# Performance work log

Hardware: AMD Instinct MI355X
Metric: run time of the kernel (lower is better)

Reference implementation:

```python
import math
import jax, jax.numpy as jnp
import numpy as np

HIDDEN = 1024
HEADS = 16
HEAD_DIM = HIDDEN // HEADS  # 64
SEQ = 4096
PATCH = 4064  # num rotated (patch) tokens; last PATCH positions get RoPE
EPS = 1e-6


def setup_inputs() -> dict:
    key = jax.random.key(0)
    ks = jax.random.split(key, 8)
    return {
        "x": jax.random.normal(ks[0], (1, SEQ, HIDDEN), dtype=jnp.float32),
        "rope_cos": jax.random.uniform(ks[1], (PATCH, HEAD_DIM // 2), dtype=jnp.float32),
        "rope_sin": jax.random.uniform(ks[2], (PATCH, HEAD_DIM // 2), dtype=jnp.float32),
        "wq": jax.random.normal(ks[3], (HIDDEN, HIDDEN), dtype=jnp.float32) / math.sqrt(HIDDEN),
        "wk": jax.random.normal(ks[4], (HIDDEN, HIDDEN), dtype=jnp.float32) / math.sqrt(HIDDEN),
        "wv": jax.random.normal(ks[5], (HIDDEN, HIDDEN), dtype=jnp.float32) / math.sqrt(HIDDEN),
        "wo": jax.random.normal(ks[6], (HIDDEN, HIDDEN), dtype=jnp.float32) / math.sqrt(HIDDEN),
        "q_norm_w": jnp.ones((HEAD_DIM,), dtype=jnp.float32),
        "k_norm_w": jnp.ones((HEAD_DIM,), dtype=jnp.float32),
    }


def _rms_norm(t, w):
    # RMSNorm over the last (head_dim) axis
    return t * jax.lax.rsqrt(jnp.mean(t * t, axis=-1, keepdims=True) + EPS) * w


def _apply_rope(t, cos, sin):
    # t: [b, s, h, d]; rotate only the last PATCH positions, pairwise complex mul
    b, s, h, d = t.shape
    P = cos.shape[0]
    tail = t[:, s - P:].reshape(b, P, h, d // 2, 2)
    x0, x1 = tail[..., 0], tail[..., 1]
    c = cos[None, :, None, :]
    sn = sin[None, :, None, :]
    rot = jnp.stack([x0 * c - x1 * sn, x0 * sn + x1 * c], axis=-1).reshape(b, P, h, d)
    return jnp.concatenate([t[:, : s - P], rot], axis=1)


def reference(x, rope_cos, rope_sin, wq, wk, wv, wo, q_norm_w, k_norm_w):
    b, s, _ = x.shape
    q = (x @ wq.T).reshape(b, s, HEADS, HEAD_DIM)
    k = (x @ wk.T).reshape(b, s, HEADS, HEAD_DIM)
    v = (x @ wv.T).reshape(b, s, HEADS, HEAD_DIM)
    q = _rms_norm(q, q_norm_w)
    k = _rms_norm(k, k_norm_w)
    q = _apply_rope(q, rope_cos, rope_sin)
    k = _apply_rope(k, rope_cos, rope_sin)
    q = q / math.sqrt(HEAD_DIM)
    scores = jnp.einsum('bqhd,bkhd->bhqk', q, k)
    attn = jax.nn.softmax(scores.astype(jnp.float32), axis=-1)
    out = jnp.einsum('bhqk,bkhd->bqhd', attn, v).reshape(b, s, HIDDEN)
    return out @ wo.T
```

## Files before the change

### kernel.cpp

```cpp
#include <hip/hip_runtime.h>
#include <hip/hip_bf16.h>
#include <stdint.h>

#define HIDDEN 1024
#define HEADS 16
#define HEAD_DIM 64
#define SEQ 4096
#define PATCH 4064
#define SKIP 32

typedef __attribute__((ext_vector_type(8))) short bf16x8;
typedef __attribute__((ext_vector_type(4))) float f32x4;
typedef __attribute__((ext_vector_type(2))) float f32x2;
typedef __attribute__((ext_vector_type(16))) float f32x16;

__device__ __forceinline__ float b2f(unsigned short u){
  union{uint32_t i; float f;} c; c.i = ((uint32_t)u)<<16; return c.f;
}
__device__ __forceinline__ unsigned short f2b(float f){
  union{float f; uint32_t i;} c; c.f=f;
  uint32_t r = c.i + 0x7fffu + ((c.i>>16)&1u);
  return (unsigned short)(r>>16);
}
__device__ __forceinline__ uint32_t cvtpk(float a, float b){
  uint32_t r;
  asm("v_cvt_pk_bf16_f32 %0, %1, %2" : "=v"(r) : "v"(a), "v"(b));
  return r;
}

#define GLD16(gp, lp) __builtin_amdgcn_global_load_lds( \
    (const __attribute__((address_space(1))) void*)(gp), \
    (__attribute__((address_space(3))) void*)(lp), 16, 0, 0)

__global__ __launch_bounds__(256) void convert_all(
    const float* __restrict__ x,  const float* __restrict__ wq,
    const float* __restrict__ wk, const float* __restrict__ wv,
    const float* __restrict__ wo,
    unsigned short* __restrict__ xb,  unsigned short* __restrict__ wqb,
    unsigned short* __restrict__ wkb, unsigned short* __restrict__ wvb,
    unsigned short* __restrict__ wob)
{
  size_t u = (size_t)blockIdx.x*256 + threadIdx.x;
  size_t e = u*8;
  const float* src; unsigned short* dst; size_t off;
  if      (e < 4194304ull) { src=x;  dst=xb;  off=e;            }
  else if (e < 5242880ull) { src=wq; dst=wqb; off=e-4194304ull; }
  else if (e < 6291456ull) { src=wk; dst=wkb; off=e-5242880ull; }
  else if (e < 7340032ull) { src=wv; dst=wvb; off=e-6291456ull; }
  else                     { src=wo; dst=wob; off=e-7340032ull; }
  float4 v0 = *(const float4*)(src+off);
  float4 v1 = *(const float4*)(src+off+4);
  union { bf16x8 v; unsigned short h[8]; } o;
  o.h[0]=f2b(v0.x); o.h[1]=f2b(v0.y); o.h[2]=f2b(v0.z); o.h[3]=f2b(v0.w);
  o.h[4]=f2b(v1.x); o.h[5]=f2b(v1.y); o.h[6]=f2b(v1.z); o.h[7]=f2b(v1.w);
  *(bf16x8*)(dst+off) = o.v;
}

__global__ __launch_bounds__(256) void gemm_qkv(
    const unsigned short* __restrict__ A,
    const unsigned short* __restrict__ B0,
    const unsigned short* __restrict__ B1,
    const unsigned short* __restrict__ B2,
    unsigned short* __restrict__ qout, unsigned short* __restrict__ kout,
    unsigned short* __restrict__ vout,
    const float* __restrict__ rc, const float* __restrict__ rs,
    const float* __restrict__ qw, const float* __restrict__ kw,
    int M, int Nper, int K)
{
  __shared__ unsigned short smem[16384];
  const int tid = threadIdx.x;
  const int w = tid>>6, l = tid&63;
  const int wm = w>>1, wn = w&1;
  const int g = l>>4, lr = l&15;
  const int bm = blockIdx.x;
  int bn = blockIdx.y;
  const int tilesPer = Nper >> 7;
  const int sel = bn / tilesPer;
  bn -= sel*tilesPer;
  const unsigned short* Bsel = (sel==0) ? B0 : ((sel==1) ? B1 : B2);

  const int off0 = w*1024 + l*16;
  const int r0 = off0>>6, c0 = (off0&63)>>1;
  const int off1 = off0 + 4096;
  const int r1 = off1>>6, c1 = (off1&63)>>1;

  const unsigned short* Ab = A    + (size_t)(bm*128)*K;
  const unsigned short* Bb = Bsel + (size_t)(bn*128)*K;

#define STG(db, kt) do { \
    GLD16(Ab + (size_t)r0*K + (kt) + c0, (char*)smem + (db) + off0); \
    GLD16(Ab + (size_t)r1*K + (kt) + c1, (char*)smem + (db) + off1); \
    GLD16(Bb + (size_t)r0*K + (kt) + c0, (char*)smem + (db) + 8192 + off0); \
    GLD16(Bb + (size_t)r1*K + (kt) + c1, (char*)smem + (db) + 8192 + off1); } while(0)

  f32x4 zero = {0.f,0.f,0.f,0.f};
  f32x4 acc[4][4];
  #pragma unroll
  for (int m=0;m<4;m++)
    #pragma unroll
    for (int n=0;n<4;n++) acc[m][n]=zero;

  const int nkt = K >> 5;
  STG(0, 0);
  for (int t = 0; t < nkt; ++t) {
    __syncthreads();
    const int db = (t&1)<<14;
    if (t+1 < nkt) STG(db^16384, (t+1)*32);
    bf16x8 a[4], b[4];
    #pragma unroll
    for (int m=0;m<4;m++)
      a[m] = *(const bf16x8*)((char*)smem + db + (wm*64 + m*16 + lr)*64 + g*16);
    #pragma unroll
    for (int n=0;n<4;n++)
      b[n] = *(const bf16x8*)((char*)smem + db + 8192 + (wn*64 + n*16 + lr)*64 + g*16);
    #pragma unroll
    for (int m=0;m<4;m++)
      #pragma unroll
      for (int n=0;n<4;n++)
        acc[m][n] = __builtin_amdgcn_mfma_f32_16x16x32_bf16(a[m], b[n], acc[m][n], 0,0,0);
  }
#undef STG

  if (sel <= 1) {
    const float* nw = (sel==0) ? qw : kw;
    unsigned short* dst = (sel==0) ? qout : kout;
    const float scl = (sel==0) ? 0.18033688011112042f : 1.0f;
    float wl[4];
    #pragma unroll
    for (int n=0;n<4;n++) wl[n] = nw[n*16+lr];
    const int hglob = bn*2 + wn;
    #pragma unroll
    for (int m=0;m<4;m++){
      const int rowb = bm*128 + wm*64 + m*16 + g*4;
      float rn[4];
      #pragma unroll
      for (int r=0;r<4;r++){
        float ss = 0.f;
        #pragma unroll
        for (int n=0;n<4;n++) ss += acc[m][n][r]*acc[m][n][r];
        ss += __shfl_xor(ss,1); ss += __shfl_xor(ss,2);
        ss += __shfl_xor(ss,4); ss += __shfl_xor(ss,8);
        rn[r] = rsqrtf(ss*(1.f/64.f) + 1e-6f);
      }
      #pragma unroll
      for (int r=0;r<4;r++){
        const int row = rowb + r;
        const int p = row - SKIP;
        #pragma unroll
        for (int n=0;n<4;n++){
          float v = acc[m][n][r]*rn[r]*wl[n];
          float c = 1.f, sn = 0.f;
          if (p >= 0){
            const int d2 = (n*16+lr)>>1;
            c  = rc[p*(HEAD_DIM/2) + d2];
            sn = rs[p*(HEAD_DIM/2) + d2];
          }
          const float partner = __shfl_xor(v, 1);
          const float o2 = (lr&1) ? (partner*sn + v*c) : (v*c - partner*sn);
          dst[(size_t)row*HIDDEN + hglob*64 + n*16 + lr] = f2b(o2*scl);
        }
      }
    }
  } else {
    #pragma unroll
    for (int m=0;m<4;m++){
      const int row = bm*128 + wm*64 + m*16 + g*4;
      #pragma unroll
      for (int n=0;n<4;n++){
        const int col = bn*128 + wn*64 + n*16 + lr;
        #pragma unroll
        for (int r=0;r<4;r++)
          vout[(size_t)(row+r)*HIDDEN + col] = f2b(acc[m][n][r]);
      }
    }
  }
}

__global__ __launch_bounds__(256) void gemm_out(
    const unsigned short* __restrict__ A,
    const unsigned short* __restrict__ B,
    float* __restrict__ Cf, int M, int N, int K)
{
  __shared__ unsigned short smem[12288];
  const int tid = threadIdx.x;
  const int w = tid>>6, l = tid&63;
  const int wm = w>>1, wn = w&1;
  const int g = l>>4, lr = l&15;
  const int bm = blockIdx.x;
  const int bn = blockIdx.y;

  const int off0 = w*1024 + l*16;
  const int r0 = off0>>6, c0 = (off0&63)>>1;
  const int off1 = off0 + 4096;
  const int r1 = off1>>6, c1 = (off1&63)>>1;
  const int offB = tid*16;
  const int rB = offB>>6, cB = (offB&63)>>1;

  const unsigned short* Ab = A + (size_t)(bm*128)*K;
  const unsigned short* Bb = B + (size_t)(bn*64)*K;

#define STG(db, kt) do { \
    GLD16(Ab + (size_t)r0*K + (kt) + c0, (char*)smem + (db) + off0); \
    GLD16(Ab + (size_t)r1*K + (kt) + c1, (char*)smem + (db) + off1); \
    GLD16(Bb + (size_t)rB*K + (kt) + cB, (char*)smem + (db) + 8192 + offB); } while(0)

  f32x4 zero = {0.f,0.f,0.f,0.f};
  f32x4 acc[4][2];
  #pragma unroll
  for (int m=0;m<4;m++)
    #pragma unroll
    for (int n=0;n<2;n++) acc[m][n]=zero;

  const int nkt = K >> 5;
  STG(0, 0);
  for (int t = 0; t < nkt; ++t) {
    __syncthreads();
    const int db = (t&1)*12288;
    if (t+1 < nkt) STG(db^12288, (t+1)*32);
    bf16x8 a[4], b[2];
    #pragma unroll
    for (int m=0;m<4;m++)
      a[m] = *(const bf16x8*)((char*)smem + db + (wm*64 + m*16 + lr)*64 + g*16);
    #pragma unroll
    for (int n=0;n<2;n++)
      b[n] = *(const bf16x8*)((char*)smem + db + 8192 + (wn*32 + n*16 + lr)*64 + g*16);
    #pragma unroll
    for (int m=0;m<4;m++)
      #pragma unroll
      for (int n=0;n<2;n++)
        acc[m][n] = __builtin_amdgcn_mfma_f32_16x16x32_bf16(a[m], b[n], acc[m][n], 0,0,0);
  }
#undef STG

  #pragma unroll
  for (int m=0;m<4;m++){
    const int row = bm*128 + wm*64 + m*16 + g*4;
    #pragma unroll
    for (int n=0;n<2;n++){
      const int col = bn*64 + wn*32 + n*16 + lr;
      #pragma unroll
      for (int r=0;r<4;r++)
        Cf[(size_t)(row+r)*N + col] = acc[m][n][r];
    }
  }
}

__global__ __launch_bounds__(256) void transpose_v(
    const unsigned short* __restrict__ v, unsigned short* __restrict__ vt)
{
  __shared__ unsigned short t[64*72];
  const int h = blockIdx.y;
  const int s0 = blockIdx.x * 64;
  const int tid = threadIdx.x;
  #pragma unroll
  for (int i=0;i<2;i++){
    const int e = tid + i*256;
    const int r = e>>3, cc = (e&7)*8;
    *(bf16x8*)&t[r*72+cc] = *(const bf16x8*)(v + (size_t)(s0+r)*HIDDEN + h*HEAD_DIM + cc);
  }
  __syncthreads();
  #pragma unroll
  for (int i=0;i<2;i++){
    const int e = tid + i*256;
    const int d = e>>3, sc = (e&7)*8;
    union { bf16x8 v8; unsigned short h8[8]; } o;
    #pragma unroll
    for (int j=0;j<8;j++){
      const int x  = sc + j;
      const int px = (x & ~12) | ((x&4)<<1) | ((x&8)>>1);
      o.h8[j] = t[px*72 + d];
    }
    *(bf16x8*)(vt + (size_t)(h*HEAD_DIM + d)*SEQ + s0 + sc) = o.v8;
  }
}

__device__ __forceinline__ void softmax_pack(f32x16 (&st)[2], f32x2 &lacc, bf16x8 (&pf)[4]){
  float pv[32];
  #pragma unroll
  for (int i=0;i<16;i++){
    pv[i]    = __builtin_amdgcn_exp2f(st[0][i]);
    pv[16+i] = __builtin_amdgcn_exp2f(st[1][i]);
  }
  #pragma unroll
  for (int i=0;i<8;i++){
    f32x2 a; a.x = pv[2*i];    a.y = pv[2*i+1];    lacc += a;
    f32x2 b; b.x = pv[16+2*i]; b.y = pv[16+2*i+1]; lacc += b;
  }
  #pragma unroll
  for (int t2=0; t2<2; t2++)
    #pragma unroll
    for (int e=0; e<2; e++){
      union { uint32_t u4[4]; bf16x8 v8; } pu;
      #pragma unroll
      for (int u=0; u<4; u++)
        pu.u4[u] = cvtpk(pv[t2*16+e*8+2*u], pv[t2*16+e*8+2*u+1]);
      pf[2*t2+e] = pu.v8;
    }
}

__global__ __launch_bounds__(256, 2) void attn_kernel(
    const unsigned short* __restrict__ q, const unsigned short* __restrict__ k,
    const unsigned short* __restrict__ vt, unsigned short* __restrict__ po,
    float* __restrict__ lbuf)
{
  __shared__ unsigned short smem[32768];
  const int fid = blockIdx.x + 16*(blockIdx.y + 16*blockIdx.z);
  const int h    = (fid&7)*2 + ((fid>>3)&1);
  const int rem  = fid>>4;
  const int q0   = (rem&15)*256;
  const int half = rem>>4;
  const int tid = threadIdx.x;
  const int w = tid>>6, l = tid&63;
  const int hi = l>>5, lo = l&31;
  const int NT = SEQ/128/2;
  const int tbase = half * NT;

  int kcol[4], vcol[4], vrow[4];
  #pragma unroll
  for (int i=0;i<4;i++){
    const int c = tid + i*256;
    const int rk = c>>3;
    kcol[i] = ((c&7)*16) ^ ((rk&7)<<4);
    const int rv = c>>4;
    vrow[i] = rv;
    vcol[i] = (((c&7)*16) ^ ((rv&7)<<4)) + ((c>>3)&1)*128;
  }
  const unsigned short* kPtr[4]; const unsigned short* vPtr[4];
  #pragma unroll
  for (int i=0;i<4;i++){
    kPtr[i] = k  + (size_t)((tid + i*256)>>3)*HIDDEN + h*HEAD_DIM + (kcol[i]>>1);
    vPtr[i] = vt + ((size_t)(h*HEAD_DIM + vrow[i]))*SEQ + (vcol[i]>>1);
  }

#define STAGE(b, kOffE, vOffE) do { \
    GLD16(kPtr[0] + (kOffE), (char*)smem + (b)*32768 + (tid      )*16); \
    GLD16(kPtr[1] + (kOffE), (char*)smem + (b)*32768 + (tid+ 256 )*16); \
    GLD16(kPtr[2] + (kOffE), (char*)smem + (b)*32768 + (tid+ 512 )*16); \
    GLD16(kPtr[3] + (kOffE), (char*)smem + (b)*32768 + (tid+ 768 )*16); \
    GLD16(vPtr[0] + (vOffE), (char*)smem + (b)*32768 + 16384 + (tid      )*16); \
    GLD16(vPtr[1] + (vOffE), (char*)smem + (b)*32768 + 16384 + (tid+ 256 )*16); \
    GLD16(vPtr[2] + (vOffE), (char*)smem + (b)*32768 + 16384 + (tid+ 512 )*16); \
    GLD16(vPtr[3] + (vOffE), (char*)smem + (b)*32768 + 16384 + (tid+ 768 )*16); \
  } while(0)

  const int swz = (lo&7)<<4;
  int colo[4];
  #pragma unroll
  for (int ks=0; ks<4; ks++) colo[ks] = ((2*ks+hi)*16) ^ swz;

  bf16x8 qf0[4], qf1[4];
  {
    const unsigned short* qp = q + (size_t)(q0 + w*64 + lo)*HIDDEN + h*HEAD_DIM;
    #pragma unroll
    for (int ks=0; ks<4; ks++){
      qf0[ks] = *(const bf16x8*)(qp + ks*16 + hi*8);
      qf1[ks] = *(const bf16x8*)(qp + 32*HIDDEN + ks*16 + hi*8);
    }
  }

  f32x16 ot0[2], ot1[2];
  #pragma unroll
  for (int m2=0;m2<2;m2++)
    #pragma unroll
    for (int i=0;i<16;i++){ ot0[m2][i] = 0.f; ot1[m2][i] = 0.f; }
  f32x2 lacc0 = {0.f,0.f}, lacc1 = {0.f,0.f};

  STAGE(0, (size_t)tbase*128*HIDDEN, (size_t)tbase*128);

  for (int t = 0; t < NT; ++t) {
    __syncthreads();
    if (t+1 < NT) {
      const size_t ta = (size_t)(tbase + t + 1);
      STAGE((t+1)&1, ta*128*HIDDEN, ta*128);
    }
    const char* Kb = (const char*)smem + (t&1)*32768;
    const char* Vb = Kb + 16384;

    f32x16 sA0[2], sA1[2], sB0[2], sB1[2];
    __builtin_amdgcn_s_setprio(1);
    #pragma unroll
    for (int c=0;c<2;c++){
      #pragma unroll
      for (int i=0;i<16;i++){ sA0[c][i]=0.f; sA1[c][i]=0.f; sB0[c][i]=0.f; sB1[c][i]=0.f; }
      #pragma unroll
      for (int ks=0; ks<4; ks++){
        bf16x8 a0 = *(const bf16x8*)(Kb + (32*c+lo)*128 + colo[ks]);
        sA0[c] = __builtin_amdgcn_mfma_f32_32x32x16_bf16(a0, qf0[ks], sA0[c], 0,0,0);
        sA1[c] = __builtin_amdgcn_mfma_f32_32x32x16_bf16(a0, qf1[ks], sA1[c], 0,0,0);
      }
      #pragma unroll
      for (int ks=0; ks<4; ks++){
        bf16x8 a1 = *(const bf16x8*)(Kb + 8192 + (32*c+lo)*128 + colo[ks]);
        sB0[c] = __builtin_amdgcn_mfma_f32_32x32x16_bf16(a1, qf0[ks], sB0[c], 0,0,0);
        sB1[c] = __builtin_amdgcn_mfma_f32_32x32x16_bf16(a1, qf1[ks], sB1[c], 0,0,0);
      }
    }
    __builtin_amdgcn_s_setprio(0);

    bf16x8 pf0[4], pf1[4];
    softmax_pack(sA0, lacc0, pf0);
    softmax_pack(sA1, lacc1, pf1);

    __builtin_amdgcn_s_setprio(1);
    #pragma unroll
    for (int m2=0;m2<2;m2++)
      #pragma unroll
      for (int ks=0; ks<4; ks++){
        bf16x8 a = *(const bf16x8*)(Vb + (32*m2+lo)*256 + colo[ks]);
        ot0[m2] = __builtin_amdgcn_mfma_f32_32x32x16_bf16(a, pf0[ks], ot0[m2], 0,0,0);
        ot1[m2] = __builtin_amdgcn_mfma_f32_32x32x16_bf16(a, pf1[ks], ot1[m2], 0,0,0);
      }
    __builtin_amdgcn_s_setprio(0);

    bf16x8 pg0[4], pg1[4];
    softmax_pack(sB0, lacc0, pg0);
    softmax_pack(sB1, lacc1, pg1);

    __builtin_amdgcn_s_setprio(1);
    #pragma unroll
    for (int m2=0;m2<2;m2++)
      #pragma unroll
      for (int ks=0; ks<4; ks++){
        bf16x8 a = *(const bf16x8*)(Vb + (32*m2+lo)*256 + 128 + colo[ks]);
        ot0[m2] = __builtin_amdgcn_mfma_f32_32x32x16_bf16(a, pg0[ks], ot0[m2], 0,0,0);
        ot1[m2] = __builtin_amdgcn_mfma_f32_32x32x16_bf16(a, pg1[ks], ot1[m2], 0,0,0);
      }
    __builtin_amdgcn_s_setprio(0);
  }

  {
    float ls0 = lacc0.x + lacc0.y;
    ls0 += __shfl_xor(ls0, 32);
    float ls1 = lacc1.x + lacc1.y;
    ls1 += __shfl_xor(ls1, 32);
    if (hi == 0){
      lbuf[(size_t)half*HEADS*SEQ + h*SEQ + q0 + w*64 + lo]      = ls0;
      lbuf[(size_t)half*HEADS*SEQ + h*SEQ + q0 + w*64 + 32 + lo] = ls1;
    }
  }

  __syncthreads();
  #pragma unroll
  for (int m2=0;m2<2;m2++)
    #pragma unroll
    for (int f=0; f<4; f++)
      #pragma unroll
      for (int u=0; u<2; u++){
        const int d = 32*m2 + 8*f + 4*hi + 2*u;
        const uint32_t w0 = cvtpk(ot0[m2][4*f+2*u], ot0[m2][4*f+2*u+1]);
        *(uint32_t*)((char*)smem + (w*64+lo)*128 + ((d*2) ^ swz)) = w0;
        const uint32_t w1 = cvtpk(ot1[m2][4*f+2*u], ot1[m2][4*f+2*u+1]);
        *(uint32_t*)((char*)smem + (w*64+32+lo)*128 + ((d*2) ^ swz)) = w1;
      }
  __syncthreads();
  unsigned short* pout = po + (size_t)half*SEQ*HIDDEN;
  #pragma unroll
  for (int rr=0; rr<2; rr++){
    const int ql = rr*128 + (tid>>1), xh = tid&1;
    #pragma unroll
    for (int i=0;i<4;i++){
      const int cb = xh*64 + i*16;
      bf16x8 vv = *(const bf16x8*)((const char*)smem + ql*128 + (cb ^ ((ql&7)<<4)));
      *(bf16x8*)(pout + (size_t)(q0+ql)*HIDDEN + h*HEAD_DIM + (cb>>1)) = vv;
    }
  }
#undef STAGE
}

__global__ __launch_bounds__(256) void combine_halves(
    const unsigned short* __restrict__ po, const float* __restrict__ lbuf,
    unsigned short* __restrict__ at)
{
  const size_t e = ((size_t)blockIdx.x*256 + threadIdx.x)*8;
  const int qrow = (int)(e >> 10);
  const int h = (int)((e >> 6) & 15);
  const float li = 1.0f / (lbuf[h*SEQ + qrow] + lbuf[HEADS*SEQ + h*SEQ + qrow]);
  union { bf16x8 v; unsigned short s[8]; } a, b, o;
  a.v = *(const bf16x8*)(po + e);
  b.v = *(const bf16x8*)(po + (size_t)SEQ*HIDDEN + e);
  #pragma unroll
  for (int j=0;j<8;j++)
    o.s[j] = f2b((b2f(a.s[j]) + b2f(b.s[j])) * li);
  *(bf16x8*)(at + e) = o.v;
}

extern "C" void kernel_launch(void* const* d_in, const int* in_sizes, int n_in,
                              void* d_out, int out_size, void* d_ws, size_t ws_size,
                              hipStream_t stream)
{
  const float* x  = (const float*)d_in[0];
  const float* rc = (const float*)d_in[1];
  const float* rs = (const float*)d_in[2];
  const float* wq = (const float*)d_in[3];
  const float* wk = (const float*)d_in[4];
  const float* wv = (const float*)d_in[5];
  const float* wo = (const float*)d_in[6];
  const float* qw = (const float*)d_in[7];
  const float* kw = (const float*)d_in[8];
  float* out = (float*)d_out;

  char* ws = (char*)d_ws;
  const size_t MB = 1024*1024;
  unsigned short* xb  = (unsigned short*)(ws + 0);
  unsigned short* wqb = (unsigned short*)(ws + 8*MB);
  unsigned short* wkb = (unsigned short*)(ws + 10*MB);
  unsigned short* wvb = (unsigned short*)(ws + 12*MB);
  unsigned short* wob = (unsigned short*)(ws + 14*MB);
  unsigned short* qkv = (unsigned short*)(ws + 16*MB);
  unsigned short* qb = qkv;
  unsigned short* kb = qkv + (size_t)SEQ*HIDDEN;
  unsigned short* vb = qkv + (size_t)2*SEQ*HIDDEN;
  unsigned short* vt = (unsigned short*)(ws + 0);
  float*          lbuf = (float*)(ws + 8*MB);
  unsigned short* po = (unsigned short*)(ws + 32*MB);
  unsigned short* at = (unsigned short*)(ws + 40*MB);

  convert_all<<<4096, 256, 0, stream>>>(x, wq, wk, wv, wo, xb, wqb, wkb, wvb, wob);
  gemm_qkv<<<dim3(32,24), 256, 0, stream>>>(
      xb, wqb, wkb, wvb, qb, kb, vb, rc, rs, qw, kw, SEQ, HIDDEN, HIDDEN);
  transpose_v<<<dim3(64,16), 256, 0, stream>>>(vb, vt);
  attn_kernel<<<dim3(16,16,2), 256, 0, stream>>>(qb, kb, vt, po, lbuf);
  combine_halves<<<2048, 256, 0, stream>>>(po, lbuf, at);
  gemm_out<<<dim3(32,16), 256, 0, stream>>>(at, wob, out, SEQ, HIDDEN, HIDDEN);
}
```

Before: 174.2 us.

## Split KV halves within one 512-thread block and combine in shared memory

The attention kernel now runs both key-sequence halves inside a single 512-thread workgroup. Each 256-thread half streams 64-key tiles through its own double buffer, and the two partial outputs and row sums are merged through LDS. This removes the separate combine_halves launch and the global round trip for the partial outputs and row sums. In exchange, the grid halves to 256 workgroups at one block per CU, and the per-iteration tile shrinks from 128 to 64 keys, which doubles the number of barriers per key processed.

```diff
diff --git a/kernel.cpp b/kernel.cpp
--- a/kernel.cpp
+++ b/kernel.cpp
@@ -298,49 +298,38 @@
     }
 }
 
-__global__ __launch_bounds__(256, 2) void attn_kernel(
+__global__ __launch_bounds__(512, 1) void attn_kernel(
     const unsigned short* __restrict__ q, const unsigned short* __restrict__ k,
-    const unsigned short* __restrict__ vt, unsigned short* __restrict__ po,
-    float* __restrict__ lbuf)
+    const unsigned short* __restrict__ vt, unsigned short* __restrict__ at)
 {
   __shared__ unsigned short smem[32768];
-  const int fid = blockIdx.x + 16*(blockIdx.y + 16*blockIdx.z);
-  const int h    = (fid&7)*2 + ((fid>>3)&1);
-  const int rem  = fid>>4;
-  const int q0   = (rem&15)*256;
-  const int half = rem>>4;
+  __shared__ float lsm[512];
+  const int fid = blockIdx.x + 16*blockIdx.y;
+  const int h  = (fid&7)*2 + ((fid>>3)&1);
+  const int q0 = (fid>>4)*256;
   const int tid = threadIdx.x;
-  const int w = tid>>6, l = tid&63;
+  const int half = tid>>8;
+  const int ht = tid&255;
+  const int w = (tid>>6)&3, l = tid&63;
   const int hi = l>>5, lo = l&31;
-  const int NT = SEQ/128/2;
-  const int tbase = half * NT;
-
-  int kcol[4], vcol[4], vrow[4];
-  #pragma unroll
-  for (int i=0;i<4;i++){
-    const int c = tid + i*256;
-    const int rk = c>>3;
-    kcol[i] = ((c&7)*16) ^ ((rk&7)<<4);
-    const int rv = c>>4;
-    vrow[i] = rv;
-    vcol[i] = (((c&7)*16) ^ ((rv&7)<<4)) + ((c>>3)&1)*128;
-  }
-  const unsigned short* kPtr[4]; const unsigned short* vPtr[4];
-  #pragma unroll
-  for (int i=0;i<4;i++){
-    kPtr[i] = k  + (size_t)((tid + i*256)>>3)*HIDDEN + h*HEAD_DIM + (kcol[i]>>1);
-    vPtr[i] = vt + ((size_t)(h*HEAD_DIM + vrow[i]))*SEQ + (vcol[i]>>1);
-  }
+  const int NT = 32;
+  const int tbase = half*NT;
+  const int hbase = half*32768;
+
+  const int cA = ht, cB = ht + 256;
+  const int rA = cA>>3, rB = cB>>3;
+  const int colA = ((cA&7)*16) ^ ((rA&7)<<4);
+  const int colB = ((cB&7)*16) ^ ((rB&7)<<4);
+  const unsigned short* kA = k  + (size_t)rA*HIDDEN + h*HEAD_DIM + (colA>>1);
+  const unsigned short* kB = k  + (size_t)rB*HIDDEN + h*HEAD_DIM + (colB>>1);
+  const unsigned short* vA = vt + ((size_t)(h*HEAD_DIM + rA))*SEQ + (colA>>1);
+  const unsigned short* vB = vt + ((size_t)(h*HEAD_DIM + rB))*SEQ + (colB>>1);
 
 #define STAGE(b, kOffE, vOffE) do { \
-    GLD16(kPtr[0] + (kOffE), (char*)smem + (b)*32768 + (tid      )*16); \
-    GLD16(kPtr[1] + (kOffE), (char*)smem + (b)*32768 + (tid+ 256 )*16); \
-    GLD16(kPtr[2] + (kOffE), (char*)smem + (b)*32768 + (tid+ 512 )*16); \
-    GLD16(kPtr[3] + (kOffE), (char*)smem + (b)*32768 + (tid+ 768 )*16); \
-    GLD16(vPtr[0] + (vOffE), (char*)smem + (b)*32768 + 16384 + (tid      )*16); \
-    GLD16(vPtr[1] + (vOffE), (char*)smem + (b)*32768 + 16384 + (tid+ 256 )*16); \
-    GLD16(vPtr[2] + (vOffE), (char*)smem + (b)*32768 + 16384 + (tid+ 512 )*16); \
-    GLD16(vPtr[3] + (vOffE), (char*)smem + (b)*32768 + 16384 + (tid+ 768 )*16); \
+    GLD16(kA + (kOffE), (char*)smem + hbase + (b)*16384 + cA*16); \
+    GLD16(kB + (kOffE), (char*)smem + hbase + (b)*16384 + cB*16); \
+    GLD16(vA + (vOffE), (char*)smem + hbase + (b)*16384 + 8192 + cA*16); \
+    GLD16(vB + (vOffE), (char*)smem + hbase + (b)*16384 + 8192 + cB*16); \
   } while(0)
 
   const int swz = (lo&7)<<4;
@@ -365,81 +354,58 @@
     for (int i=0;i<16;i++){ ot0[m2][i] = 0.f; ot1[m2][i] = 0.f; }
   f32x2 lacc0 = {0.f,0.f}, lacc1 = {0.f,0.f};
 
-  STAGE(0, (size_t)tbase*128*HIDDEN, (size_t)tbase*128);
+  STAGE(0, (size_t)tbase*64*HIDDEN, (size_t)tbase*64);
 
   for (int t = 0; t < NT; ++t) {
     __syncthreads();
     if (t+1 < NT) {
       const size_t ta = (size_t)(tbase + t + 1);
-      STAGE((t+1)&1, ta*128*HIDDEN, ta*128);
-    }
-    const char* Kb = (const char*)smem + (t&1)*32768;
-    const char* Vb = Kb + 16384;
-
-    f32x16 sA0[2], sA1[2], sB0[2], sB1[2];
+      STAGE((t+1)&1, ta*64*HIDDEN, ta*64);
+    }
+    const char* Kb = (const char*)smem + hbase + (t&1)*16384;
+    const char* Vb = Kb + 8192;
+
+    f32x16 st0[2], st1[2];
     __builtin_amdgcn_s_setprio(1);
     #pragma unroll
     for (int c=0;c<2;c++){
       #pragma unroll
-      for (int i=0;i<16;i++){ sA0[c][i]=0.f; sA1[c][i]=0.f; sB0[c][i]=0.f; sB1[c][i]=0.f; }
+      for (int i=0;i<16;i++){ st0[c][i] = 0.f; st1[c][i] = 0.f; }
       #pragma unroll
       for (int ks=0; ks<4; ks++){
-        bf16x8 a0 = *(const bf16x8*)(Kb + (32*c+lo)*128 + colo[ks]);
-        sA0[c] = __builtin_amdgcn_mfma_f32_32x32x16_bf16(a0, qf0[ks], sA0[c], 0,0,0);
-        sA1[c] = __builtin_amdgcn_mfma_f32_32x32x16_bf16(a0, qf1[ks], sA1[c], 0,0,0);
-      }
+        bf16x8 a = *(const bf16x8*)(Kb + (32*c+lo)*128 + colo[ks]);
+        st0[c] = __builtin_amdgcn_mfma_f32_32x32x16_bf16(a, qf0[ks], st0[c], 0,0,0);
+        st1[c] = __builtin_amdgcn_mfma_f32_32x32x16_bf16(a, qf1[ks], st1[c], 0,0,0);
+      }
+    }
+    __builtin_amdgcn_s_setprio(0);
+
+    bf16x8 pf0[4], pf1[4];
+    softmax_pack(st0, lacc0, pf0);
+    softmax_pack(st1, lacc1, pf1);
+
+    __builtin_amdgcn_s_setprio(1);
+    #pragma unroll
+    for (int m2=0;m2<2;m2++)
       #pragma unroll
       for (int ks=0; ks<4; ks++){
-        bf16x8 a1 = *(const bf16x8*)(Kb + 8192 + (32*c+lo)*128 + colo[ks]);
-        sB0[c] = __builtin_amdgcn_mfma_f32_32x32x16_bf16(a1, qf0[ks], sB0[c], 0,0,0);
-        sB1[c] = __builtin_amdgcn_mfma_f32_32x32x16_bf16(a1, qf1[ks], sB1[c], 0,0,0);
-      }
-    }
-    __builtin_amdgcn_s_setprio(0);
-
-    bf16x8 pf0[4], pf1[4];
-    softmax_pack(sA0, lacc0, pf0);
-    softmax_pack(sA1, lacc1, pf1);
-
-    __builtin_amdgcn_s_setprio(1);
-    #pragma unroll
-    for (int m2=0;m2<2;m2++)
-      #pragma unroll
-      for (int ks=0; ks<4; ks++){
-        bf16x8 a = *(const bf16x8*)(Vb + (32*m2+lo)*256 + colo[ks]);
+        bf16x8 a = *(const bf16x8*)(Vb + (32*m2+lo)*128 + colo[ks]);
         ot0[m2] = __builtin_amdgcn_mfma_f32_32x32x16_bf16(a, pf0[ks], ot0[m2], 0,0,0);
         ot1[m2] = __builtin_amdgcn_mfma_f32_32x32x16_bf16(a, pf1[ks], ot1[m2], 0,0,0);
       }
     __builtin_amdgcn_s_setprio(0);
-
-    bf16x8 pg0[4], pg1[4];
-    softmax_pack(sB0, lacc0, pg0);
-    softmax_pack(sB1, lacc1, pg1);
-
-    __builtin_amdgcn_s_setprio(1);
-    #pragma unroll
-    for (int m2=0;m2<2;m2++)
-      #pragma unroll
-      for (int ks=0; ks<4; ks++){
-        bf16x8 a = *(const bf16x8*)(Vb + (32*m2+lo)*256 + 128 + colo[ks]);
-        ot0[m2] = __builtin_amdgcn_mfma_f32_32x32x16_bf16(a, pg0[ks], ot0[m2], 0,0,0);
-        ot1[m2] = __builtin_amdgcn_mfma_f32_32x32x16_bf16(a, pg1[ks], ot1[m2], 0,0,0);
-      }
-    __builtin_amdgcn_s_setprio(0);
-  }
-
-  {
-    float ls0 = lacc0.x + lacc0.y;
-    ls0 += __shfl_xor(ls0, 32);
-    float ls1 = lacc1.x + lacc1.y;
-    ls1 += __shfl_xor(ls1, 32);
-    if (hi == 0){
-      lbuf[(size_t)half*HEADS*SEQ + h*SEQ + q0 + w*64 + lo]      = ls0;
-      lbuf[(size_t)half*HEADS*SEQ + h*SEQ + q0 + w*64 + 32 + lo] = ls1;
-    }
-  }
+  }
+
+  float ls0 = lacc0.x + lacc0.y;
+  ls0 += __shfl_xor(ls0, 32);
+  float ls1 = lacc1.x + lacc1.y;
+  ls1 += __shfl_xor(ls1, 32);
 
   __syncthreads();
+  if (hi == 0){
+    lsm[half*256 + w*64 + lo]      = ls0;
+    lsm[half*256 + w*64 + 32 + lo] = ls1;
+  }
   #pragma unroll
   for (int m2=0;m2<2;m2++)
     #pragma unroll
@@ -448,40 +414,29 @@
       for (int u=0; u<2; u++){
         const int d = 32*m2 + 8*f + 4*hi + 2*u;
         const uint32_t w0 = cvtpk(ot0[m2][4*f+2*u], ot0[m2][4*f+2*u+1]);
-        *(uint32_t*)((char*)smem + (w*64+lo)*128 + ((d*2) ^ swz)) = w0;
+        *(uint32_t*)((char*)smem + hbase + (w*64+lo)*128 + ((d*2) ^ swz)) = w0;
         const uint32_t w1 = cvtpk(ot1[m2][4*f+2*u], ot1[m2][4*f+2*u+1]);
-        *(uint32_t*)((char*)smem + (w*64+32+lo)*128 + ((d*2) ^ swz)) = w1;
+        *(uint32_t*)((char*)smem + hbase + (w*64+32+lo)*128 + ((d*2) ^ swz)) = w1;
       }
   __syncthreads();
-  unsigned short* pout = po + (size_t)half*SEQ*HIDDEN;
-  #pragma unroll
-  for (int rr=0; rr<2; rr++){
-    const int ql = rr*128 + (tid>>1), xh = tid&1;
+
+  {
+    const int ql = tid>>1, xh = tid&1;
+    const float li = 1.0f / (lsm[ql] + lsm[256 + ql]);
     #pragma unroll
     for (int i=0;i<4;i++){
       const int cb = xh*64 + i*16;
-      bf16x8 vv = *(const bf16x8*)((const char*)smem + ql*128 + (cb ^ ((ql&7)<<4)));
-      *(bf16x8*)(pout + (size_t)(q0+ql)*HIDDEN + h*HEAD_DIM + (cb>>1)) = vv;
+      const int off = ql*128 + (cb ^ ((ql&7)<<4));
+      union { bf16x8 v; unsigned short s[8]; } a, b, o;
+      a.v = *(const bf16x8*)((const char*)smem + off);
+      b.v = *(const bf16x8*)((const char*)smem + 32768 + off);
+      #pragma unroll
+      for (int j=0;j<8;j++)
+        o.s[j] = f2b((b2f(a.s[j]) + b2f(b.s[j])) * li);
+      *(bf16x8*)(at + (size_t)(q0+ql)*HIDDEN + h*HEAD_DIM + (cb>>1)) = o.v;
     }
   }
 #undef STAGE
-}
-
-__global__ __launch_bounds__(256) void combine_halves(
-    const unsigned short* __restrict__ po, const float* __restrict__ lbuf,
-    unsigned short* __restrict__ at)
-{
-  const size_t e = ((size_t)blockIdx.x*256 + threadIdx.x)*8;
-  const int qrow = (int)(e >> 10);
-  const int h = (int)((e >> 6) & 15);
-  const float li = 1.0f / (lbuf[h*SEQ + qrow] + lbuf[HEADS*SEQ + h*SEQ + qrow]);
-  union { bf16x8 v; unsigned short s[8]; } a, b, o;
-  a.v = *(const bf16x8*)(po + e);
-  b.v = *(const bf16x8*)(po + (size_t)SEQ*HIDDEN + e);
-  #pragma unroll
-  for (int j=0;j<8;j++)
-    o.s[j] = f2b((b2f(a.s[j]) + b2f(b.s[j])) * li);
-  *(bf16x8*)(at + e) = o.v;
 }
 
 extern "C" void kernel_launch(void* const* d_in, const int* in_sizes, int n_in,
@@ -511,15 +466,12 @@
   unsigned short* kb = qkv + (size_t)SEQ*HIDDEN;
   unsigned short* vb = qkv + (size_t)2*SEQ*HIDDEN;
   unsigned short* vt = (unsigned short*)(ws + 0);
-  float*          lbuf = (float*)(ws + 8*MB);
-  unsigned short* po = (unsigned short*)(ws + 32*MB);
   unsigned short* at = (unsigned short*)(ws + 40*MB);
 
   convert_all<<<4096, 256, 0, stream>>>(x, wq, wk, wv, wo, xb, wqb, wkb, wvb, wob);
   gemm_qkv<<<dim3(32,24), 256, 0, stream>>>(
       xb, wqb, wkb, wvb, qb, kb, vb, rc, rs, qw, kw, SEQ, HIDDEN, HIDDEN);
   transpose_v<<<dim3(64,16), 256, 0, stream>>>(vb, vt);
-  attn_kernel<<<dim3(16,16,2), 256, 0, stream>>>(qb, kb, vt, po, lbuf);
-  combine_halves<<<2048, 256, 0, stream>>>(po, lbuf, at);
+  attn_kernel<<<dim3(16,16), 512, 0, stream>>>(qb, kb, vt, at);
   gemm_out<<<dim3(32,16), 256, 0, stream>>>(at, wob, out, SEQ, HIDDEN, HIDDEN);
 }
```

Result: faster. 150.1 us (-13.9%).
